# Performance work log

Measured on AMD Instinct MI355X. Metric: run time of the kernel, lower is better.

The kernel has to match this reference:

```python
import jax, jax.numpy as jnp
import numpy as np

S, B, D = 2048, 1, 4096
H, HKV, DH = 32, 8, 128
THETA = 10000.0


def _rope_tables(seq_len, dim, theta):
    inv_freq = 1.0 / (theta ** (jnp.arange(0, dim, 2, dtype=jnp.float32) / dim))
    freqs = jnp.arange(seq_len, dtype=jnp.float32)[:, None] * inv_freq[None, :]  # [S, DH/2]
    return jnp.cos(freqs), jnp.sin(freqs)


def _apply_rope(x, cos, sin):
    # x: [B, H, S, DH]; non-interleaved (flash_attn interleaved=False) rotation
    half = x.shape[-1] // 2
    x1, x2 = x[..., :half], x[..., half:]
    c = cos[None, None, :, :]
    s = sin[None, None, :, :]
    return jnp.concatenate([x1 * c - x2 * s, x2 * c + x1 * s], axis=-1)


def setup_inputs() -> dict:
    key = jax.random.key(0)
    k1, k2, k3 = jax.random.split(key, 3)
    hidden_states = jax.random.normal(k1, (S, B, D), dtype=jnp.float32)
    W_qkv = jax.random.normal(k2, (D, (H + 2 * HKV) * DH), dtype=jnp.float32) * 0.02
    W_o = jax.random.normal(k3, (H * DH, D), dtype=jnp.float32) * 0.02
    sequence_mask = jnp.ones((B, S), dtype=jnp.int32)
    return {"hidden_states": hidden_states, "sequence_mask": sequence_mask,
            "W_qkv": W_qkv, "W_o": W_o}


def reference(hidden_states, sequence_mask, W_qkv, W_o):
    s, b, _ = hidden_states.shape
    qkv = hidden_states @ W_qkv  # [S, B, (H+2*HKV)*DH]
    q, k, v = jnp.split(qkv, [H * DH, H * DH + HKV * DH], axis=-1)
    q = q.reshape(s, b, H, DH).transpose(1, 2, 0, 3)    # [B, H, S, DH]
    k = k.reshape(s, b, HKV, DH).transpose(1, 2, 0, 3)  # [B, HKV, S, DH]
    v = v.reshape(s, b, HKV, DH).transpose(1, 2, 0, 3)

    cos, sin = _rope_tables(s, DH, THETA)
    q = _apply_rope(q, cos, sin)
    k = _apply_rope(k, cos, sin)

    # GQA: repeat kv heads
    rep = H // HKV
    k = jnp.repeat(k, rep, axis=1)  # [B, H, S, DH]
    v = jnp.repeat(v, rep, axis=1)

    scale = 1.0 / jnp.sqrt(jnp.asarray(DH, dtype=q.dtype))
    scores = jnp.einsum('bhqd,bhkd->bhqk', q, k) * scale
    causal = jnp.tril(jnp.ones((s, s), dtype=bool))
    scores = jnp.where(causal[None, None, :, :], scores, jnp.finfo(scores.dtype).min)
    attn = jax.nn.softmax(scores, axis=-1)
    ctx = jnp.einsum('bhqk,bhkd->bhqd', attn, v)  # [B, H, S, DH]
    ctx = ctx.transpose(2, 0, 1, 3).reshape(s, b, H * DH)  # [S, B, H*DH]
    out = ctx @ W_o  # [S, B, D]
    return out
```

## Files before the change

kernel.cpp:

```cpp
#include <hip/hip_runtime.h>

typedef unsigned short u16;
typedef __bf16 bf16x8 __attribute__((ext_vector_type(8)));
typedef float f32x4 __attribute__((ext_vector_type(4)));
typedef u16 u16x4 __attribute__((ext_vector_type(4)));

constexpr int SEQ = 2048;
constexpr int NQKV = 6144;

__device__ __forceinline__ float bf2f(u16 x) {
    unsigned int u = ((unsigned int)x) << 16;
    return __builtin_bit_cast(float, u);
}
__device__ __forceinline__ u16 f2bf(float f) {
    unsigned int u = __builtin_bit_cast(unsigned int, f);
    u += 0x7FFF + ((u >> 16) & 1);
    return (u16)(u >> 16);
}

__device__ __forceinline__ void gload16(const void* g, void* l) {
    void* gg = const_cast<void*>(g);
    __builtin_amdgcn_global_load_lds(
        (__attribute__((address_space(1))) void*)gg,
        (__attribute__((address_space(3))) void*)l, 16, 0, 0);
}

__device__ __forceinline__ void gatebar(int G) {
    if (G == 4) asm volatile("s_waitcnt vmcnt(4)" ::: "memory");
    else if (G == 3) asm volatile("s_waitcnt vmcnt(3)" ::: "memory");
    else if (G == 2) asm volatile("s_waitcnt vmcnt(2)" ::: "memory");
    else asm volatile("s_waitcnt vmcnt(0)" ::: "memory");
    __builtin_amdgcn_sched_barrier(0);
    __builtin_amdgcn_s_barrier();
    __builtin_amdgcn_sched_barrier(0);
}

__global__ void rope_table_k(float* __restrict__ tab) {
    int idx = blockIdx.x * 256 + threadIdx.x;
    if (idx >= SEQ * 64) return;
    int s = idx >> 6;
    int i = idx & 63;
    float invf = expf(-(float)i * (float)(1.0 / 64.0) * logf(10000.0f));
    float ang = (float)s * invf;
    float sv, cv;
    sincosf(ang, &sv, &cv);
    tab[idx * 2] = cv;
    tab[idx * 2 + 1] = sv;
}

__global__ __launch_bounds__(256) void cast_k(const float* __restrict__ src,
                                              u16* __restrict__ dst, int n4) {
    int i = blockIdx.x * 256 + threadIdx.x;
    if (i >= n4) return;
    f32x4 v = *(const f32x4*)&src[(size_t)i * 4];
    u16x4 o;
#pragma unroll
    for (int j = 0; j < 4; ++j) o[j] = f2bf(v[j]);
    *(u16x4*)&dst[(size_t)i * 4] = o;
}

__global__ __launch_bounds__(256) void transpose_cast_k(const float* __restrict__ src,
                                                        u16* __restrict__ dst, int R, int C) {
    __shared__ u16 tile[64][65];
    int t = threadIdx.x;
    int bx = blockIdx.x, by = blockIdx.y;
    int r0 = by * 64, c0 = bx * 64;
#pragma unroll
    for (int it = 0; it < 4; ++it) {
        int row = it * 16 + (t >> 4);
        int col = (t & 15) * 4;
        f32x4 v = *(const f32x4*)&src[(size_t)(r0 + row) * C + c0 + col];
        tile[row][col] = f2bf(v[0]); tile[row][col + 1] = f2bf(v[1]);
        tile[row][col + 2] = f2bf(v[2]); tile[row][col + 3] = f2bf(v[3]);
    }
    __syncthreads();
#pragma unroll
    for (int it = 0; it < 4; ++it) {
        int orow = it * 16 + (t >> 4);
        int ocol = (t & 15) * 4;
        u16x4 v;
        v[0] = tile[ocol][orow]; v[1] = tile[ocol + 1][orow];
        v[2] = tile[ocol + 2][orow]; v[3] = tile[ocol + 3][orow];
        *(u16x4*)&dst[(size_t)(c0 + orow) * R + r0 + ocol] = v;
    }
}

__global__ __launch_bounds__(512, 2) void gemm1_big_k(const u16* __restrict__ A,
                                                      const u16* __restrict__ BT,
                                                      u16* __restrict__ C) {
    constexpr int K = 4096, N = 6144;
    constexpr int SBUF = 57344;
    __shared__ alignas(16) char lds[2 * SBUF];

    int t = threadIdx.x;
    int lane = t & 63, w = t >> 6;
    int wr = w >> 2, wc = w & 3;
    int l15 = lane & 15, l4 = lane >> 4;

    int wg = blockIdx.x;
    int xcd = wg & 7, j = wg >> 3;
    int bm = ((xcd >> 2) << 2) + (j >> 3);
    int bn = ((xcd & 3) << 3) + (j & 7);

    const u16* Ab = A + (size_t)bm * 256 * K;
    const u16* Bb = BT + (size_t)bn * 192 * K;

    const u16* ga[4]; int da[4];
#pragma unroll
    for (int i = 0; i < 4; ++i) {
        int c = t + i * 512;
        int row = c >> 3;
        int ch = (c & 7) ^ (row & 7);
        ga[i] = Ab + (size_t)row * K + ch * 8;
        da[i] = c * 16;
    }
    const u16* gb[3]; int db[3];
#pragma unroll
    for (int i = 0; i < 3; ++i) {
        int c = t + i * 512;
        int row = c >> 3;
        int ch = (c & 7) ^ (row & 7);
        gb[i] = Bb + (size_t)row * K + ch * 8;
        db[i] = 32768 + c * 16;
    }

    auto stage = [&](int kt) {
        char* L = lds + (kt & 1) * SBUF;
        int ko = kt * 64;
#pragma unroll
        for (int i = 0; i < 4; ++i) gload16(ga[i] + ko, L + da[i]);
#pragma unroll
        for (int i = 0; i < 3; ++i) gload16(gb[i] + ko, L + db[i]);
    };

    f32x4 acc[8][3];
#pragma unroll
    for (int i = 0; i < 8; ++i)
#pragma unroll
        for (int j2 = 0; j2 < 3; ++j2) acc[i][j2] = f32x4{0.f, 0.f, 0.f, 0.f};

    int arow[8];
#pragma unroll
    for (int fm = 0; fm < 8; ++fm) arow[fm] = wr * 128 + fm * 16 + l15;
    int brow[3];
#pragma unroll
    for (int fn = 0; fn < 3; ++fn) brow[fn] = wc * 48 + fn * 16 + l15;

    stage(0);
    gatebar(0);

    for (int kt = 0; kt < 64; ++kt) {
        const u16* L = (const u16*)(lds + (kt & 1) * SBUF);
        if (kt + 1 < 64) stage(kt + 1);
        bf16x8 bf[3][2];
#pragma unroll
        for (int fn = 0; fn < 3; ++fn)
#pragma unroll
            for (int kk = 0; kk < 2; ++kk) {
                int ch = (kk * 4 + l4) ^ (brow[fn] & 7);
                bf[fn][kk] = *(const bf16x8*)&L[16384 + brow[fn] * 64 + ch * 8];
            }
#pragma unroll
        for (int p = 0; p < 4; ++p) {
            bf16x8 af[2][2];
#pragma unroll
            for (int f2 = 0; f2 < 2; ++f2)
#pragma unroll
                for (int kk = 0; kk < 2; ++kk) {
                    int r = arow[p * 2 + f2];
                    int ch = (kk * 4 + l4) ^ (r & 7);
                    af[f2][kk] = *(const bf16x8*)&L[r * 64 + ch * 8];
                }
            __builtin_amdgcn_s_setprio(1);
#pragma unroll
            for (int f2 = 0; f2 < 2; ++f2)
#pragma unroll
                for (int kk = 0; kk < 2; ++kk)
#pragma unroll
                    for (int fn = 0; fn < 3; ++fn)
                        acc[p * 2 + f2][fn] = __builtin_amdgcn_mfma_f32_16x16x32_bf16(
                            af[f2][kk], bf[fn][kk], acc[p * 2 + f2][fn], 0, 0, 0);
            __builtin_amdgcn_s_setprio(0);
        }
        gatebar(0);
    }

#pragma unroll
    for (int fm = 0; fm < 8; ++fm)
#pragma unroll
        for (int fn = 0; fn < 3; ++fn)
#pragma unroll
            for (int i = 0; i < 4; ++i) {
                int row = bm * 256 + wr * 128 + fm * 16 + l4 * 4 + i;
                int col = bn * 192 + wc * 48 + fn * 16 + l15;
                C[(size_t)row * N + col] = f2bf(acc[fm][fn][i]);
            }
}

template <int NF, bool F32OUT>
__global__ __launch_bounds__(512, 4) void gemm_pipe_k(const u16* __restrict__ A,
                                                      const u16* __restrict__ BT,
                                                      void* __restrict__ Cv, int N, int K) {
    constexpr int BN = NF * 64;
    constexpr int SA = 128 * 64;
    constexpr int SB = BN * 64;
    constexpr int SBUF = SA + SB;
    __shared__ alignas(16) char lds[3 * SBUF];

    int t = threadIdx.x;
    int lane = t & 63, w = t >> 6;
    int wr = w >> 2, wc = w & 3;
    int l15 = lane & 15, l4 = lane >> 4;

    int wg = blockIdx.x;
    int xcd = wg & 7, j = wg >> 3;
    int bm = ((xcd >> 2) << 3) + (j >> 3);
    int bn = ((xcd & 3) << 3) + (j & 7);

    const u16* Ab = A + (size_t)bm * 128 * K;
    const u16* Bb = BT + (size_t)bn * BN * K;

    int ar = t >> 2;
    int akc = (t & 3) ^ ((ar >> 1) & 3);
    const u16* ga = Ab + (size_t)ar * K + akc * 8;
    int br0 = t >> 2;
    int bk0 = (t & 3) ^ ((br0 >> 1) & 3);
    const u16* gb0 = Bb + (size_t)br0 * K + bk0 * 8;
    int bc1 = 512 + t;
    int br1 = bc1 >> 2;
    int bk1 = (bc1 & 3) ^ ((br1 >> 1) & 3);
    const u16* gb1 = Bb + (size_t)br1 * K + bk1 * 8;
    bool hasB1 = (NF == 3) && (w < 4);
    int myG = (NF == 3) ? ((w < 4) ? 3 : 2) : 2;

    auto stage = [&](int v) {
        int b = v - (v / 3) * 3;
        char* LA = lds + b * SBUF;
        char* LB = LA + SA;
        int ko = v * 32;
        gload16(ga + ko, LA + t * 16);
        gload16(gb0 + ko, LB + t * 16);
        if (NF == 3) {
            if (hasB1) gload16(gb1 + ko, LB + bc1 * 16);
        }
    };

    f32x4 acc[4][NF];
#pragma unroll
    for (int i = 0; i < 4; ++i)
#pragma unroll
        for (int j2 = 0; j2 < NF; ++j2) acc[i][j2] = f32x4{0.f, 0.f, 0.f, 0.f};

    int arow[4], akk[4];
#pragma unroll
    for (int fm = 0; fm < 4; ++fm) {
        arow[fm] = wr * 64 + fm * 16 + l15;
        akk[fm] = l4 ^ ((arow[fm] >> 1) & 3);
    }
    int brow[NF], bkk[NF];
#pragma unroll
    for (int fn = 0; fn < NF; ++fn) {
        brow[fn] = wc * (NF * 16) + fn * 16 + l15;
        bkk[fn] = l4 ^ ((brow[fn] >> 1) & 3);
    }

    int nk = K >> 5;
    stage(0);
    stage(1);
    gatebar(myG);

    int b = 0;
    for (int v = 0; v < nk; ++v) {
        const u16* LA = (const u16*)(lds + b * SBUF);
        const u16* LB = LA + SA / 2;
        if (v + 2 < nk) stage(v + 2);
        bf16x8 bf[NF];
#pragma unroll
        for (int fn = 0; fn < NF; ++fn)
            bf[fn] = *(const bf16x8*)&LB[brow[fn] * 32 + bkk[fn] * 8];
        __builtin_amdgcn_s_setprio(1);
#pragma unroll
        for (int fm = 0; fm < 4; ++fm) {
            bf16x8 af = *(const bf16x8*)&LA[arow[fm] * 32 + akk[fm] * 8];
#pragma unroll
            for (int fn = 0; fn < NF; ++fn)
                acc[fm][fn] = __builtin_amdgcn_mfma_f32_16x16x32_bf16(af, bf[fn],
                                                                     acc[fm][fn], 0, 0, 0);
        }
        __builtin_amdgcn_s_setprio(0);
        if (v < nk - 1) gatebar((v + 2 < nk) ? myG : 0);
        b = (b == 2) ? 0 : b + 1;
    }

#pragma unroll
    for (int fm = 0; fm < 4; ++fm)
#pragma unroll
        for (int fn = 0; fn < NF; ++fn)
#pragma unroll
            for (int i = 0; i < 4; ++i) {
                int row = bm * 128 + wr * 64 + fm * 16 + l4 * 4 + i;
                int col = bn * BN + wc * (NF * 16) + fn * 16 + l15;
                if constexpr (F32OUT)
                    ((float*)Cv)[(size_t)row * N + col] = acc[fm][fn][i];
                else
                    ((u16*)Cv)[(size_t)row * N + col] = f2bf(acc[fm][fn][i]);
            }
}

__global__ __launch_bounds__(256) void repack_rope_k(const u16* __restrict__ QKV,
                                                     const float* __restrict__ tab,
                                                     u16* __restrict__ Qo, u16* __restrict__ Ko,
                                                     u16* __restrict__ Vo) {
    int idx = blockIdx.x * 256 + threadIdx.x;
    int i4 = (idx & 15) * 4;
    int su = idx >> 4;
    int u = su % 48;
    int s = su / 48;
    if (u < 40) {
        const float* tp = tab + (s * 64 + i4) * 2;
        f32x4 t0 = *(const f32x4*)tp;
        f32x4 t1 = *(const f32x4*)(tp + 4);
        float cv[4] = {t0[0], t0[2], t1[0], t1[2]};
        float sv[4] = {t0[1], t0[3], t1[1], t1[3]};
        const u16* base;
        u16* ob;
        if (u < 32) {
            base = QKV + (size_t)s * NQKV + u * 128;
            ob = Qo + ((size_t)u * SEQ + s) * 128;
        } else {
            base = QKV + (size_t)s * NQKV + 4096 + (u - 32) * 128;
            ob = Ko + ((size_t)(u - 32) * SEQ + s) * 128;
        }
        u16x4 x1 = *(const u16x4*)(base + i4);
        u16x4 x2 = *(const u16x4*)(base + 64 + i4);
        u16x4 o1, o2;
#pragma unroll
        for (int j = 0; j < 4; ++j) {
            float a = bf2f(x1[j]), b = bf2f(x2[j]);
            o1[j] = f2bf(a * cv[j] - b * sv[j]);
            o2[j] = f2bf(b * cv[j] + a * sv[j]);
        }
        *(u16x4*)(ob + i4) = o1;
        *(u16x4*)(ob + 64 + i4) = o2;
    } else {
        int hv = u - 40;
        const u16* base = QKV + (size_t)s * NQKV + 5120 + hv * 128;
        u16* ob = Vo + ((size_t)hv * SEQ + s) * 128;
        *(u16x4*)(ob + i4) = *(const u16x4*)(base + i4);
        *(u16x4*)(ob + 64 + i4) = *(const u16x4*)(base + 64 + i4);
    }
}

__global__ __launch_bounds__(512) void attn_k(const u16* __restrict__ Qg,
                                              const u16* __restrict__ Kg,
                                              const u16* __restrict__ Vg,
                                              u16* __restrict__ ctx) {
    constexpr float SCL2 = 0.08838834764831845f * 1.44269504088896340736f;
    constexpr float THR = 11.5f;
    __shared__ alignas(16) u16 Klds[2][64 * 128];
    __shared__ alignas(16) u16 VT[2][128 * 72];
    __shared__ alignas(16) u16 Plds[8 * 16 * 72];

    int t = threadIdx.x;
    int lane = t & 63, w = t >> 6;
    int l15 = lane & 15, l4 = lane >> 4;
    int bx = blockIdx.x;
    int h = blockIdx.y, hkv = h >> 2;
    const u16* Kh = Kg + (size_t)hkv * SEQ * 128;
    const u16* Vh = Vg + (size_t)hkv * SEQ * 128;
    u16* Pw = &Plds[w * 1152];

    int kr[2], kchs[2];
#pragma unroll
    for (int i2 = 0; i2 < 2; ++i2) {
        int c = t + i2 * 512;
        kr[i2] = c >> 4;
        kchs[i2] = (c & 15) ^ (kr[i2] & 7);
    }
    int vr = lane, vcb = (t >> 6) * 16;

    int q0 = bx * 128;
    int ntA = 2 * bx + 2;

    bf16x8 qf[4], vreg[2];
    f32x4 o[8];
    float m_i[4], l_i[4];

    auto kvbase = [&](int tt) { return (tt < ntA ? tt : tt - ntA) << 6; };
    auto load_q = [&]() {
        const u16* Qh = Qg + ((size_t)h * SEQ + q0 + w * 16 + l15) * 128;
#pragma unroll
        for (int ks = 0; ks < 4; ++ks) qf[ks] = *(const bf16x8*)(Qh + ks * 32 + l4 * 8);
    };
    auto reset_acc = [&]() {
#pragma unroll
        for (int nf = 0; nf < 8; ++nf) o[nf] = f32x4{0.f, 0.f, 0.f, 0.f};
#pragma unroll
        for (int i = 0; i < 4; ++i) { m_i[i] = -3.0e38f; l_i[i] = 0.f; }
    };
    auto write_ctx = [&]() {
        float inv[4];
#pragma unroll
        for (int i = 0; i < 4; ++i) {
            float rs = l_i[i];
            rs += __shfl_xor(rs, 1);
            rs += __shfl_xor(rs, 2);
            rs += __shfl_xor(rs, 4);
            rs += __shfl_xor(rs, 8);
            inv[i] = 1.0f / rs;
        }
#pragma unroll
        for (int nf = 0; nf < 8; ++nf)
#pragma unroll
            for (int i = 0; i < 4; ++i) {
                int qrow = q0 + w * 16 + l4 * 4 + i;
                ctx[(size_t)qrow * 4096 + h * 128 + nf * 16 + l15] = f2bf(o[nf][i] * inv[i]);
            }
    };
    auto loadV = [&](int tt) {
        const u16* Vt = Vh + (size_t)kvbase(tt) * 128;
#pragma unroll
        for (int seg = 0; seg < 2; ++seg)
            vreg[seg] = *(const bf16x8*)(Vt + (size_t)vr * 128 + vcb + seg * 8);
    };
    auto stageK = [&](int tt) {
        const u16* Kt = Kh + (size_t)kvbase(tt) * 128;
        char* kb = (char*)Klds[tt & 1];
#pragma unroll
        for (int i2 = 0; i2 < 2; ++i2)
            gload16(Kt + kr[i2] * 128 + kchs[i2] * 8, kb + (size_t)(t + i2 * 512) * 16);
    };
    auto writeV = [&](int tt) {
        u16* vb = VT[tt & 1];
#pragma unroll
        for (int seg = 0; seg < 2; ++seg) {
            int c0 = vcb + seg * 8;
            u16* vv = (u16*)&vreg[seg];
#pragma unroll
            for (int j = 0; j < 8; ++j) vb[(c0 + j) * 72 + vr] = vv[j];
        }
    };

    load_q();
    reset_acc();
    loadV(0);
    stageK(0);
    asm volatile("s_waitcnt vmcnt(0)" ::: "memory");
    __builtin_amdgcn_sched_barrier(0);
    writeV(0);

    for (int tt = 0; tt < 34; ++tt) {
        asm volatile("s_waitcnt lgkmcnt(0)" ::: "memory");
        __builtin_amdgcn_sched_barrier(0);
        __builtin_amdgcn_s_barrier();
        __builtin_amdgcn_sched_barrier(0);
        bool nxt = (tt + 1 < 34);
        if (nxt) {
            loadV(tt + 1);
            stageK(tt + 1);
        }
        gatebar(nxt ? 4 : 0);
        if (tt == ntA) {
            write_ctx();
            q0 = (15 - bx) * 128;
            load_q();
            reset_acc();
        }

        int b = tt & 1;
        int kv0 = kvbase(tt);
        const u16* KL = Klds[b];

        f32x4 sa[4];
#pragma unroll
        for (int cg = 0; cg < 4; ++cg) {
            sa[cg] = f32x4{0.f, 0.f, 0.f, 0.f};
            int row = cg * 16 + l15;
#pragma unroll
            for (int ks = 0; ks < 4; ++ks) {
                int chs = (ks * 4 + l4) ^ (row & 7);
                bf16x8 kf = *(const bf16x8*)&KL[row * 128 + chs * 8];
                sa[cg] = __builtin_amdgcn_mfma_f32_16x16x32_bf16(qf[ks], kf, sa[cg], 0, 0, 0);
            }
        }
#pragma unroll
        for (int cg = 0; cg < 4; ++cg)
#pragma unroll
            for (int i = 0; i < 4; ++i) sa[cg][i] *= SCL2;
        if (kv0 + 63 > q0 + w * 16) {
#pragma unroll
            for (int cg = 0; cg < 4; ++cg) {
                int col = kv0 + cg * 16 + l15;
#pragma unroll
                for (int i = 0; i < 4; ++i) {
                    int qrow = q0 + w * 16 + l4 * 4 + i;
                    if (col > qrow) sa[cg][i] = -3.0e38f;
                }
            }
        }
        float lmx[4];
#pragma unroll
        for (int i = 0; i < 4; ++i)
            lmx[i] = fmaxf(fmaxf(sa[0][i], sa[1][i]), fmaxf(sa[2][i], sa[3][i]));
        bool defer = __all((lmx[0] <= m_i[0] + THR) & (lmx[1] <= m_i[1] + THR) &
                           (lmx[2] <= m_i[2] + THR) & (lmx[3] <= m_i[3] + THR));
        if (!defer) {
            float corr[4];
#pragma unroll
            for (int i = 0; i < 4; ++i) {
                float m0 = lmx[i];
                m0 = fmaxf(m0, __shfl_xor(m0, 1));
                m0 = fmaxf(m0, __shfl_xor(m0, 2));
                m0 = fmaxf(m0, __shfl_xor(m0, 4));
                m0 = fmaxf(m0, __shfl_xor(m0, 8));
                float mnew = fmaxf(m_i[i], m0);
                corr[i] = __builtin_amdgcn_exp2f(m_i[i] - mnew);
                m_i[i] = mnew;
                l_i[i] *= corr[i];
            }
#pragma unroll
            for (int nf = 0; nf < 8; ++nf) {
                o[nf][0] *= corr[0]; o[nf][1] *= corr[1];
                o[nf][2] *= corr[2]; o[nf][3] *= corr[3];
            }
        }
        if (nxt) writeV(tt + 1);
#pragma unroll
        for (int i = 0; i < 4; ++i) {
            int prow = l4 * 4 + i;
            int sw = (prow >> 1) & 3;
            float rs = 0.f;
#pragma unroll
            for (int cg = 0; cg < 4; ++cg) {
                float p = __builtin_amdgcn_exp2f(sa[cg][i] - m_i[i]);
                rs += p;
                int ch = cg * 2 + (l15 >> 3);
                Pw[prow * 72 + ((ch ^ sw) << 3) + (l15 & 7)] = f2bf(p);
            }
            l_i[i] += rs;
        }
        asm volatile("s_waitcnt lgkmcnt(0)" ::: "memory");
        __builtin_amdgcn_sched_barrier(0);
#pragma unroll
        for (int kst = 0; kst < 2; ++kst) {
            int pchs = (kst * 4 + l4) ^ ((l15 >> 1) & 3);
            bf16x8 pf = *(const bf16x8*)&Pw[l15 * 72 + pchs * 8];
#pragma unroll
            for (int nf = 0; nf < 8; ++nf) {
                bf16x8 vf = *(const bf16x8*)&VT[b][(nf * 16 + l15) * 72 + kst * 32 + l4 * 8];
                o[nf] = __builtin_amdgcn_mfma_f32_16x16x32_bf16(pf, vf, o[nf], 0, 0, 0);
            }
        }
    }
    write_ctx();
}

extern "C" void kernel_launch(void* const* d_in, const int* in_sizes, int n_in,
                              void* d_out, int out_size, void* d_ws, size_t ws_size,
                              hipStream_t stream) {
    const float* hidden = (const float*)d_in[0];
    const float* Wqkv = (const float*)d_in[2];
    const float* Wo = (const float*)d_in[3];
    float* out = (float*)d_out;
    char* ws = (char*)d_ws;

    u16* WqkvT   = (u16*)(ws + 0);
    u16* Qb      = (u16*)(ws + 0);
    u16* Kb      = (u16*)(ws + 16777216);
    u16* Vb      = (u16*)(ws + 20971520);
    u16* WoT     = (u16*)(ws + 25165824);
    u16* QKV     = (u16*)(ws + 50331648);
    u16* ctx     = (u16*)(ws + 58720256);
    float* tab   = (float*)(ws + 75497472);
    u16* hiddenB = (u16*)(ws + 76546048);

    rope_table_k<<<512, 256, 0, stream>>>(tab);
    cast_k<<<8192, 256, 0, stream>>>(hidden, hiddenB, 2048 * 4096 / 4);
    transpose_cast_k<<<dim3(96, 64), 256, 0, stream>>>(Wqkv, WqkvT, 4096, 6144);
    gemm1_big_k<<<256, 512, 0, stream>>>(hiddenB, WqkvT, QKV);
    repack_rope_k<<<6144, 256, 0, stream>>>(QKV, tab, Qb, Kb, Vb);
    transpose_cast_k<<<dim3(64, 64), 256, 0, stream>>>(Wo, WoT, 4096, 4096);
    attn_k<<<dim3(8, 32), 512, 0, stream>>>(Qb, Kb, Vb, ctx);
    gemm_pipe_k<2, true><<<512, 512, 0, stream>>>(ctx, WoT, out, 4096, 4096);
}
```

Before: 334.3 us.

## Replace output projection GEMM with 256x128 tile, BK=64 double-buffered kernel

The output projection GEMM moves from a templated 128x128 tile kernel with BK=32 and triple buffering to a dedicated 256x128 tile kernel with BK=64 and double buffering, modelled on the QKV GEMM. Each block now does more MFMA work per LDS load and issues fewer barriers, and the grid drops from 512 to 256 blocks. In exchange, larger LDS and register use lowers occupancy (launch bounds 2), and the shallower pipeline may expose more load latency.

```diff
diff --git a/kernel.cpp b/kernel.cpp
--- a/kernel.cpp
+++ b/kernel.cpp
@@ -197,15 +197,12 @@
             }
 }
 
-template <int NF, bool F32OUT>
-__global__ __launch_bounds__(512, 4) void gemm_pipe_k(const u16* __restrict__ A,
+__global__ __launch_bounds__(512, 2) void gemm2_big_k(const u16* __restrict__ A,
                                                       const u16* __restrict__ BT,
-                                                      void* __restrict__ Cv, int N, int K) {
-    constexpr int BN = NF * 64;
-    constexpr int SA = 128 * 64;
-    constexpr int SB = BN * 64;
-    constexpr int SBUF = SA + SB;
-    __shared__ alignas(16) char lds[3 * SBUF];
+                                                      float* __restrict__ C) {
+    constexpr int K = 4096, N = 4096;
+    constexpr int SBUF = 49152;
+    __shared__ alignas(16) char lds[2 * SBUF];
 
     int t = threadIdx.x;
     int lane = t & 63, w = t >> 6;
@@ -214,96 +211,101 @@
 
     int wg = blockIdx.x;
     int xcd = wg & 7, j = wg >> 3;
-    int bm = ((xcd >> 2) << 3) + (j >> 3);
+    int bm = ((xcd >> 2) << 2) + (j >> 3);
     int bn = ((xcd & 3) << 3) + (j & 7);
 
-    const u16* Ab = A + (size_t)bm * 128 * K;
-    const u16* Bb = BT + (size_t)bn * BN * K;
-
-    int ar = t >> 2;
-    int akc = (t & 3) ^ ((ar >> 1) & 3);
-    const u16* ga = Ab + (size_t)ar * K + akc * 8;
-    int br0 = t >> 2;
-    int bk0 = (t & 3) ^ ((br0 >> 1) & 3);
-    const u16* gb0 = Bb + (size_t)br0 * K + bk0 * 8;
-    int bc1 = 512 + t;
-    int br1 = bc1 >> 2;
-    int bk1 = (bc1 & 3) ^ ((br1 >> 1) & 3);
-    const u16* gb1 = Bb + (size_t)br1 * K + bk1 * 8;
-    bool hasB1 = (NF == 3) && (w < 4);
-    int myG = (NF == 3) ? ((w < 4) ? 3 : 2) : 2;
-
-    auto stage = [&](int v) {
-        int b = v - (v / 3) * 3;
-        char* LA = lds + b * SBUF;
-        char* LB = LA + SA;
-        int ko = v * 32;
-        gload16(ga + ko, LA + t * 16);
-        gload16(gb0 + ko, LB + t * 16);
-        if (NF == 3) {
-            if (hasB1) gload16(gb1 + ko, LB + bc1 * 16);
-        }
-    };
-
-    f32x4 acc[4][NF];
-#pragma unroll
-    for (int i = 0; i < 4; ++i)
-#pragma unroll
-        for (int j2 = 0; j2 < NF; ++j2) acc[i][j2] = f32x4{0.f, 0.f, 0.f, 0.f};
-
-    int arow[4], akk[4];
-#pragma unroll
-    for (int fm = 0; fm < 4; ++fm) {
-        arow[fm] = wr * 64 + fm * 16 + l15;
-        akk[fm] = l4 ^ ((arow[fm] >> 1) & 3);
-    }
-    int brow[NF], bkk[NF];
-#pragma unroll
-    for (int fn = 0; fn < NF; ++fn) {
-        brow[fn] = wc * (NF * 16) + fn * 16 + l15;
-        bkk[fn] = l4 ^ ((brow[fn] >> 1) & 3);
-    }
-
-    int nk = K >> 5;
+    const u16* Ab = A + (size_t)bm * 256 * K;
+    const u16* Bb = BT + (size_t)bn * 128 * K;
+
+    const u16* ga[4]; int da[4];
+#pragma unroll
+    for (int i = 0; i < 4; ++i) {
+        int c = t + i * 512;
+        int row = c >> 3;
+        int ch = (c & 7) ^ (row & 7);
+        ga[i] = Ab + (size_t)row * K + ch * 8;
+        da[i] = c * 16;
+    }
+    const u16* gb[2]; int db[2];
+#pragma unroll
+    for (int i = 0; i < 2; ++i) {
+        int c = t + i * 512;
+        int row = c >> 3;
+        int ch = (c & 7) ^ (row & 7);
+        gb[i] = Bb + (size_t)row * K + ch * 8;
+        db[i] = 32768 + c * 16;
+    }
+
+    auto stage = [&](int kt) {
+        char* L = lds + (kt & 1) * SBUF;
+        int ko = kt * 64;
+#pragma unroll
+        for (int i = 0; i < 4; ++i) gload16(ga[i] + ko, L + da[i]);
+#pragma unroll
+        for (int i = 0; i < 2; ++i) gload16(gb[i] + ko, L + db[i]);
+    };
+
+    f32x4 acc[8][2];
+#pragma unroll
+    for (int i = 0; i < 8; ++i)
+#pragma unroll
+        for (int j2 = 0; j2 < 2; ++j2) acc[i][j2] = f32x4{0.f, 0.f, 0.f, 0.f};
+
+    int arow[8];
+#pragma unroll
+    for (int fm = 0; fm < 8; ++fm) arow[fm] = wr * 128 + fm * 16 + l15;
+    int brow[2];
+#pragma unroll
+    for (int fn = 0; fn < 2; ++fn) brow[fn] = wc * 32 + fn * 16 + l15;
+
     stage(0);
-    stage(1);
-    gatebar(myG);
-
-    int b = 0;
-    for (int v = 0; v < nk; ++v) {
-        const u16* LA = (const u16*)(lds + b * SBUF);
-        const u16* LB = LA + SA / 2;
-        if (v + 2 < nk) stage(v + 2);
-        bf16x8 bf[NF];
-#pragma unroll
-        for (int fn = 0; fn < NF; ++fn)
-            bf[fn] = *(const bf16x8*)&LB[brow[fn] * 32 + bkk[fn] * 8];
-        __builtin_amdgcn_s_setprio(1);
-#pragma unroll
-        for (int fm = 0; fm < 4; ++fm) {
-            bf16x8 af = *(const bf16x8*)&LA[arow[fm] * 32 + akk[fm] * 8];
-#pragma unroll
-            for (int fn = 0; fn < NF; ++fn)
-                acc[fm][fn] = __builtin_amdgcn_mfma_f32_16x16x32_bf16(af, bf[fn],
-                                                                     acc[fm][fn], 0, 0, 0);
-        }
-        __builtin_amdgcn_s_setprio(0);
-        if (v < nk - 1) gatebar((v + 2 < nk) ? myG : 0);
-        b = (b == 2) ? 0 : b + 1;
-    }
-
-#pragma unroll
-    for (int fm = 0; fm < 4; ++fm)
-#pragma unroll
-        for (int fn = 0; fn < NF; ++fn)
+    gatebar(0);
+
+    for (int kt = 0; kt < 64; ++kt) {
+        const u16* L = (const u16*)(lds + (kt & 1) * SBUF);
+        if (kt + 1 < 64) stage(kt + 1);
+        bf16x8 bf[2][2];
+#pragma unroll
+        for (int fn = 0; fn < 2; ++fn)
+#pragma unroll
+            for (int kk = 0; kk < 2; ++kk) {
+                int ch = (kk * 4 + l4) ^ (brow[fn] & 7);
+                bf[fn][kk] = *(const bf16x8*)&L[16384 + brow[fn] * 64 + ch * 8];
+            }
+#pragma unroll
+        for (int p = 0; p < 4; ++p) {
+            bf16x8 af[2][2];
+#pragma unroll
+            for (int f2 = 0; f2 < 2; ++f2)
+#pragma unroll
+                for (int kk = 0; kk < 2; ++kk) {
+                    int r = arow[p * 2 + f2];
+                    int ch = (kk * 4 + l4) ^ (r & 7);
+                    af[f2][kk] = *(const bf16x8*)&L[r * 64 + ch * 8];
+                }
+            __builtin_amdgcn_s_setprio(1);
+#pragma unroll
+            for (int f2 = 0; f2 < 2; ++f2)
+#pragma unroll
+                for (int kk = 0; kk < 2; ++kk)
+#pragma unroll
+                    for (int fn = 0; fn < 2; ++fn)
+                        acc[p * 2 + f2][fn] = __builtin_amdgcn_mfma_f32_16x16x32_bf16(
+                            af[f2][kk], bf[fn][kk], acc[p * 2 + f2][fn], 0, 0, 0);
+            __builtin_amdgcn_s_setprio(0);
+        }
+        gatebar(0);
+    }
+
+#pragma unroll
+    for (int fm = 0; fm < 8; ++fm)
+#pragma unroll
+        for (int fn = 0; fn < 2; ++fn)
 #pragma unroll
             for (int i = 0; i < 4; ++i) {
-                int row = bm * 128 + wr * 64 + fm * 16 + l4 * 4 + i;
-                int col = bn * BN + wc * (NF * 16) + fn * 16 + l15;
-                if constexpr (F32OUT)
-                    ((float*)Cv)[(size_t)row * N + col] = acc[fm][fn][i];
-                else
-                    ((u16*)Cv)[(size_t)row * N + col] = f2bf(acc[fm][fn][i]);
+                int row = bm * 256 + wr * 128 + fm * 16 + l4 * 4 + i;
+                int col = bn * 128 + wc * 32 + fn * 16 + l15;
+                C[(size_t)row * N + col] = acc[fm][fn][i];
             }
 }
 
@@ -581,5 +583,5 @@
     repack_rope_k<<<6144, 256, 0, stream>>>(QKV, tab, Qb, Kb, Vb);
     transpose_cast_k<<<dim3(64, 64), 256, 0, stream>>>(Wo, WoT, 4096, 4096);
     attn_k<<<dim3(8, 32), 512, 0, stream>>>(Qb, Kb, Vb, ctx);
-    gemm_pipe_k<2, true><<<512, 512, 0, stream>>>(ctx, WoT, out, 4096, 4096);
-}
+    gemm2_big_k<<<256, 512, 0, stream>>>(ctx, WoT, out);
+}
```

New measurement: 325.7 us. -2.6%, faster.
